# Kernel tuning notes

Hardware: AMD Instinct MI355X
Metric: run time of the kernel (lower is better)

The kernel has to match this reference:

```python
import jax, jax.numpy as jnp
import numpy as np

T, B, D, H, DEPTH = 256, 64, 1024, 1024, 2


def setup_inputs() -> dict:
    key = jax.random.key(0)
    ks = jax.random.split(key, 12)
    s_in = (1.0 / (D + H)) ** 0.5  # torch Linear default init scale
    s_h = (1.0 / H) ** 0.5
    qc_v = jax.random.uniform(ks[9], (DEPTH, H, H), jnp.float32, -s_h, s_h)
    # weight_norm init: g = ||v|| per output row, so initial w == v
    qc_g = jnp.linalg.norm(qc_v, axis=2)
    return {
        "inputs": jax.random.normal(ks[0], (T, B, D), jnp.float32),
        "Wf": jax.random.uniform(ks[1], (H, D + H), jnp.float32, -s_in, s_in),
        "bf": jax.random.uniform(ks[2], (H,), jnp.float32, -s_in, s_in),
        "Wi": jax.random.uniform(ks[3], (H, D + H), jnp.float32, -s_in, s_in),
        "bi": jax.random.uniform(ks[4], (H,), jnp.float32, -s_in, s_in),
        "Wu": jax.random.uniform(ks[5], (H, D + H), jnp.float32, -s_in, s_in),
        "bu": jax.random.uniform(ks[6], (H,), jnp.float32, -s_in, s_in),
        "Wo": jax.random.uniform(ks[7], (H, D + H), jnp.float32, -s_in, s_in),
        "bo": jax.random.uniform(ks[8], (H,), jnp.float32, -s_in, s_in),
        "qc_v": qc_v,
        "qc_g": qc_g,
        "qc_b": jax.random.uniform(ks[10], (DEPTH, H), jnp.float32, -s_h, s_h),
    }


def reference(inputs, Wf, bf, Wi, bi, Wu, bu, Wo, bo, qc_v, qc_g, qc_b):
    # weight_norm (dim=0): w = g * v / ||v||_row
    qc_w = qc_g[:, :, None] * qc_v / jnp.linalg.norm(qc_v, axis=2, keepdims=True)

    def qc(x):  # x: [4, B, H] -> tanh(linear) applied DEPTH times (shared across gates)
        for d in range(DEPTH):
            x = jnp.tanh(jnp.einsum('gbh,oh->gbo', x, qc_w[d]) + qc_b[d])
        return x

    h0 = jnp.zeros((inputs.shape[1], bf.shape[0]), inputs.dtype)

    def step(carry, x):
        hx, cx = carry
        comb = jnp.concatenate([x, hx], axis=1)  # [B, D+H]
        f = jax.nn.sigmoid(comb @ Wf.T + bf)
        i = jax.nn.sigmoid(comb @ Wi.T + bi)
        g = jnp.tanh(comb @ Wu.T + bu)
        o = jax.nn.sigmoid(comb @ Wo.T + bo)
        f, i, g, o = qc(jnp.stack([f, i, g, o]))
        cx = f * cx + i * g
        hx = o * jnp.tanh(cx)
        return (hx, cx), hx

    (hx, cx), outputs = jax.lax.scan(step, (h0, h0), inputs)
    return outputs, hx, cx
```

## Files before the change

kernel.cpp:

```cpp
#include <hip/hip_runtime.h>
#include <cstdint>
#include <cstddef>

typedef float f32x4 __attribute__((ext_vector_type(4)));
typedef __bf16 bf16x8 __attribute__((ext_vector_type(8)));
typedef unsigned int u32x4 __attribute__((ext_vector_type(4)));

#define T_STEPS 256
#define HD      1024
#define DHK     2048

#define LDSW_BYTES (32 * 256 * 16)
#define LDS_TOTAL  (LDSW_BYTES + 4 * 16 * 68 * 4)

__device__ __forceinline__ unsigned short f2bf(float f) {
  union { float f; unsigned u; } v; v.f = f;
  unsigned r = v.u + 0x7fffu + ((v.u >> 16) & 1u);
  return (unsigned short)(r >> 16);
}

__device__ __forceinline__ float fast_sigmoid(float x) {
  return 1.0f / (1.0f + __expf(-x));
}
__device__ __forceinline__ float fast_tanh(float x) {
  float e = __expf(2.0f * x);
  return (e - 1.0f) / (e + 1.0f);
}

__device__ __forceinline__ f32x4 mfma16(bf16x8 a, bf16x8 b, f32x4 c) {
  return __builtin_amdgcn_mfma_f32_16x16x32_bf16(a, b, c, 0, 0, 0);
}

#define LOADC(dst, vofs, base, IMM)                                            \
  asm volatile("global_load_dwordx4 %0, %1, %2 offset:" IMM " sc0 sc1"         \
               : "=v"(dst) : "v"(vofs), "s"(base) : "memory")

#define L8(st, vofs, base)                                                     \
  LOADC(st[0], vofs, base, "0");   LOADC(st[1], vofs, base, "64");             \
  LOADC(st[2], vofs, base, "128"); LOADC(st[3], vofs, base, "192");            \
  LOADC(st[4], vofs, base, "256"); LOADC(st[5], vofs, base, "320");            \
  LOADC(st[6], vofs, base, "384"); LOADC(st[7], vofs, base, "448")

#define WAITV0()                                                               \
  do { asm volatile("s_waitcnt vmcnt(0)" ::: "memory");                        \
       __builtin_amdgcn_sched_barrier(0); } while (0)

__device__ __forceinline__ void storec8(void* p, ushort4 v) {
  asm volatile("global_store_dwordx2 %0, %1, off sc0 sc1"
               :: "v"(p), "v"(v) : "memory");
}
__device__ __forceinline__ void storec2(void* p, unsigned short v) {
  unsigned vv = v;
  asm volatile("global_store_short %0, %1, off sc0 sc1"
               :: "v"(p), "v"(vv) : "memory");
}

__device__ __forceinline__ void release_flag(int* f, int v) {
  asm volatile("s_waitcnt vmcnt(0)" ::: "memory");
  __hip_atomic_store(f, v, __ATOMIC_RELAXED, __HIP_MEMORY_SCOPE_AGENT);
}
__device__ __forceinline__ void wait_ge(const int* f, int v) {
  while (__hip_atomic_load(f, __ATOMIC_RELAXED, __HIP_MEMORY_SCOPE_AGENT) < v)
    __builtin_amdgcn_s_sleep(1);
  asm volatile("" ::: "memory");
}

__global__ __launch_bounds__(256, 1) void qlstm_persist(
    const unsigned short* __restrict__ Xbf,
    const unsigned short* __restrict__ Wbf,
    const unsigned short* __restrict__ qcw,
    const float* __restrict__ bias_cat,
    const float* __restrict__ qcb,
    unsigned short* __restrict__ Gbf,
    unsigned short* __restrict__ G2bf,
    unsigned short* __restrict__ hbf,
    float* __restrict__ c_state,
    float* __restrict__ out,
    int* __restrict__ aA, int* __restrict__ aB, int* __restrict__ aC) {
  extern __shared__ char lds_raw[];
  uint4* lw = (uint4*)lds_raw;
  float* red = (float*)(lds_raw + LDSW_BYTES);

  const int nb = blockIdx.x, tid = threadIdx.x;
  const int wv = tid >> 6, lane = tid & 63;
  const int l15 = lane & 15, l16 = lane >> 4;
  const int l16o = l16 * 8;
  const int q = nb >> 6;
  const int n0 = (nb & 63) * 16;
  const int kb = wv * 256;

  {
    const unsigned short* wArow = Wbf + (size_t)(nb * 16 + l15) * DHK + kb + l16o;
    const unsigned short* wBrow = qcw + (size_t)(n0 + l15) * HD + kb + l16o;
    const unsigned short* wCrow = wBrow + (size_t)HD * HD;
#pragma unroll
    for (int s = 0; s < 8; ++s) {
      lw[s * 256 + tid]        = *(const uint4*)&wArow[s * 32];
      lw[(8 + s) * 256 + tid]  = *(const uint4*)&wArow[1024 + s * 32];
      lw[(16 + s) * 256 + tid] = *(const uint4*)&wBrow[s * 32];
      lw[(24 + s) * 256 + tid] = *(const uint4*)&wCrow[s * 32];
    }
  }
  __syncthreads();

  const int erow = tid >> 2, ecb = (tid & 3) * 4;
  const int bl = tid >> 4, cc = tid & 15;
  f32x4 biasA, biasB;
#pragma unroll
  for (int i = 0; i < 4; ++i) {
    biasA[i] = bias_cat[nb * 16 + ecb + i];
    biasB[i] = qcb[n0 + ecb + i];
  }
  const float biasC = qcb[HD + n0 + cc];

  int vofsAB[4], vofsC[4];
#pragma unroll
  for (int mt = 0; mt < 4; ++mt) {
    vofsAB[mt] = ((mt * 16 + l15) * HD + kb + l16o) * 2;
    vofsC[mt]  = ((mt * 64 + q * 16 + l15) * HD + kb + l16o) * 2;
  }
  const unsigned short* hB = hbf;
  const unsigned short* gB = Gbf + (size_t)(q * 64) * HD;

  for (int t = 0; t < T_STEPS; ++t) {
    {
      f32x4 acc[4] = {};
      const unsigned short* xb = Xbf + (size_t)t * (64 * HD);
#pragma unroll
      for (int s = 0; s < 8; ++s) {
        bf16x8 w = *(const bf16x8*)&lw[s * 256 + tid];
#pragma unroll
        for (int mt = 0; mt < 4; ++mt) {
          bf16x8 a =
              *(const bf16x8*)&xb[(size_t)(mt * 16 + l15) * HD + kb + s * 32 + l16o];
          acc[mt] = mfma16(a, w, acc[mt]);
        }
      }
      wait_ge(&aC[tid], t);
      __syncthreads();
      {
        bf16x8 st0[8], st1[8], st2[8], st3[8];
        L8(st0, vofsAB[0], hB); L8(st1, vofsAB[1], hB);
        L8(st2, vofsAB[2], hB); L8(st3, vofsAB[3], hB);
        WAITV0();
#pragma unroll
        for (int s = 0; s < 8; ++s) {
          bf16x8 w = *(const bf16x8*)&lw[(8 + s) * 256 + tid];
          acc[0] = mfma16(st0[s], w, acc[0]);
          acc[1] = mfma16(st1[s], w, acc[1]);
          acc[2] = mfma16(st2[s], w, acc[2]);
          acc[3] = mfma16(st3[s], w, acc[3]);
        }
      }
#pragma unroll
      for (int mt = 0; mt < 4; ++mt)
        *(f32x4*)&red[(wv * 16 + l15) * 68 + mt * 16 + l16 * 4] = acc[mt];
      __syncthreads();
      ushort4 pk;
#pragma unroll
      for (int i = 0; i < 4; ++i) {
        const int c = ecb + i;
        float v = red[(0 * 16 + c) * 68 + erow] + red[(1 * 16 + c) * 68 + erow] +
                  red[(2 * 16 + c) * 68 + erow] + red[(3 * 16 + c) * 68 + erow] +
                  biasA[i];
        v = (q == 2) ? fast_tanh(v) : fast_sigmoid(v);
        ((unsigned short*)&pk)[i] = f2bf(v);
      }
      storec8(&Gbf[(size_t)(q * 64 + erow) * HD + n0 + ecb], pk);
      __syncthreads();
      if (tid == 0) release_flag(&aA[nb], t + 1);
    }
    {
      if (tid < 64) wait_ge(&aA[q * 64 + tid], t + 1);
      __syncthreads();
      f32x4 acc[4] = {};
      {
        bf16x8 st0[8], st1[8], st2[8], st3[8];
        L8(st0, vofsAB[0], gB); L8(st1, vofsAB[1], gB);
        L8(st2, vofsAB[2], gB); L8(st3, vofsAB[3], gB);
        WAITV0();
#pragma unroll
        for (int s = 0; s < 8; ++s) {
          bf16x8 w = *(const bf16x8*)&lw[(16 + s) * 256 + tid];
          acc[0] = mfma16(st0[s], w, acc[0]);
          acc[1] = mfma16(st1[s], w, acc[1]);
          acc[2] = mfma16(st2[s], w, acc[2]);
          acc[3] = mfma16(st3[s], w, acc[3]);
        }
      }
#pragma unroll
      for (int mt = 0; mt < 4; ++mt)
        *(f32x4*)&red[(wv * 16 + l15) * 68 + mt * 16 + l16 * 4] = acc[mt];
      __syncthreads();
      ushort4 pk;
#pragma unroll
      for (int i = 0; i < 4; ++i) {
        const int c = ecb + i;
        float v = red[(0 * 16 + c) * 68 + erow] + red[(1 * 16 + c) * 68 + erow] +
                  red[(2 * 16 + c) * 68 + erow] + red[(3 * 16 + c) * 68 + erow] +
                  biasB[i];
        ((unsigned short*)&pk)[i] = f2bf(fast_tanh(v));
      }
      storec8(&G2bf[(size_t)(q * 64 + erow) * HD + n0 + ecb], pk);
      __syncthreads();
      if (tid == 0) release_flag(&aB[nb], t + 1);
    }
    {
      wait_ge(&aB[tid], t + 1);
      __syncthreads();
      f32x4 acc[4] = {};
      {
        bf16x8 st0[8], st1[8], st2[8], st3[8];
        L8(st0, vofsC[0], G2bf); L8(st1, vofsC[1], G2bf);
        L8(st2, vofsC[2], G2bf); L8(st3, vofsC[3], G2bf);
        WAITV0();
#pragma unroll
        for (int s = 0; s < 8; ++s) {
          bf16x8 w = *(const bf16x8*)&lw[(24 + s) * 256 + tid];
          acc[0] = mfma16(st0[s], w, acc[0]);
          acc[1] = mfma16(st1[s], w, acc[1]);
          acc[2] = mfma16(st2[s], w, acc[2]);
          acc[3] = mfma16(st3[s], w, acc[3]);
        }
      }
#pragma unroll
      for (int mt = 0; mt < 4; ++mt)
        *(f32x4*)&red[(wv * 16 + l15) * 68 + mt * 16 + l16 * 4] = acc[mt];
      __syncthreads();
      float gv[4];
#pragma unroll
      for (int g = 0; g < 4; ++g) {
        const int r = g * 16 + bl;
        float v = red[(0 * 16 + cc) * 68 + r] + red[(1 * 16 + cc) * 68 + r] +
                  red[(2 * 16 + cc) * 68 + r] + red[(3 * 16 + cc) * 68 + r] +
                  biasC;
        gv[g] = fast_tanh(v);
      }
      const int ci = (q * 16 + bl) * HD + n0 + cc;
      const float c_new = gv[0] * c_state[ci] + gv[1] * gv[2];
      const float h_new = gv[3] * fast_tanh(c_new);
      c_state[ci] = c_new;
      out[(size_t)t * (64 * HD) + ci] = h_new;
      storec2(&hbf[ci], f2bf(h_new));
      if (t == T_STEPS - 1) {
        out[(size_t)T_STEPS * (64 * HD) + ci] = h_new;
        out[(size_t)T_STEPS * (64 * HD) + 64 * HD + ci] = c_new;
      }
      __syncthreads();
      if (tid == 0) release_flag(&aC[nb], t + 1);
    }
  }
}

__global__ void xconv_kernel(const float* __restrict__ x,
                             unsigned short* __restrict__ xbf, int n4) {
  int idx = blockIdx.x * blockDim.x + threadIdx.x;
  int stride = gridDim.x * blockDim.x;
  for (int i = idx; i < n4; i += stride) {
    float4 v = ((const float4*)x)[i];
    ushort4 o;
    o.x = f2bf(v.x); o.y = f2bf(v.y); o.z = f2bf(v.z); o.w = f2bf(v.w);
    ((ushort4*)xbf)[i] = o;
  }
}

__global__ void wconv_kernel(const float* __restrict__ Wf, const float* __restrict__ Wi,
                             const float* __restrict__ Wu, const float* __restrict__ Wo,
                             const float* __restrict__ bfv, const float* __restrict__ biv,
                             const float* __restrict__ buv, const float* __restrict__ bov,
                             unsigned short* __restrict__ Wbf, float* __restrict__ bias_cat) {
  const int n = blockIdx.x;
  const int gate = n >> 10, r = n & 1023;
  const float* W = gate == 0 ? Wf : gate == 1 ? Wi : gate == 2 ? Wu : Wo;
  const float* src = W + (size_t)r * DHK;
  unsigned short* dst = Wbf + (size_t)n * DHK;
  for (int k = threadIdx.x; k < DHK; k += 256) dst[k] = f2bf(src[k]);
  if (threadIdx.x == 0) {
    const float* bsrc = gate == 0 ? bfv : gate == 1 ? biv : gate == 2 ? buv : bov;
    bias_cat[n] = bsrc[r];
  }
}

__global__ void qcw_kernel(const float* __restrict__ qcv, const float* __restrict__ qcg,
                           unsigned short* __restrict__ qcw) {
  const int row = blockIdx.x * 4 + (threadIdx.x >> 6);
  const int lane = threadIdx.x & 63;
  const float* v = qcv + (size_t)row * HD;
  float ss = 0.0f;
#pragma unroll
  for (int j = 0; j < 16; ++j) { float a = v[j * 64 + lane]; ss += a * a; }
#pragma unroll
  for (int off = 32; off > 0; off >>= 1) ss += __shfl_xor(ss, off);
  const float scale = qcg[row] / sqrtf(ss);
#pragma unroll
  for (int j = 0; j < 16; ++j)
    qcw[(size_t)row * HD + j * 64 + lane] = f2bf(v[j * 64 + lane] * scale);
}

__global__ void init_state_kernel(unsigned short* __restrict__ hbf,
                                  float* __restrict__ c_state,
                                  int* __restrict__ flags) {
  int i = blockIdx.x * blockDim.x + threadIdx.x;
  hbf[i] = 0;
  c_state[i] = 0.0f;
  if (i < 768) flags[i] = 0;
}

extern "C" void kernel_launch(void* const* d_in, const int* in_sizes, int n_in,
                              void* d_out, int out_size, void* d_ws, size_t ws_size,
                              hipStream_t stream) {
  const float* x   = (const float*)d_in[0];
  const float* Wf  = (const float*)d_in[1];
  const float* bfv = (const float*)d_in[2];
  const float* Wi  = (const float*)d_in[3];
  const float* biv = (const float*)d_in[4];
  const float* Wu  = (const float*)d_in[5];
  const float* buv = (const float*)d_in[6];
  const float* Wo  = (const float*)d_in[7];
  const float* bov = (const float*)d_in[8];
  const float* qcv = (const float*)d_in[9];
  const float* qcg = (const float*)d_in[10];
  const float* qcb = (const float*)d_in[11];
  float* out = (float*)d_out;

  char* p = (char*)d_ws;
  auto alloc = [&](size_t bytes) {
    char* r = p; p += (bytes + 255) & ~(size_t)255; return r;
  };
  unsigned short* Xbf  = (unsigned short*)alloc((size_t)T_STEPS * 64 * HD * 2);
  unsigned short* Wbf  = (unsigned short*)alloc((size_t)4096 * DHK * 2);
  unsigned short* qcw  = (unsigned short*)alloc((size_t)2 * HD * HD * 2);
  float* bias_cat      = (float*)alloc((size_t)4096 * 4);
  unsigned short* Gbf  = (unsigned short*)alloc((size_t)256 * HD * 2);
  unsigned short* G2bf = (unsigned short*)alloc((size_t)256 * HD * 2);
  unsigned short* hbf  = (unsigned short*)alloc((size_t)64 * HD * 2);
  float* c_state       = (float*)alloc((size_t)64 * HD * 4);
  int* flags           = (int*)alloc(768 * 4);

  static int lds_set = 0;
  if (!lds_set) {
    hipFuncSetAttribute((const void*)qlstm_persist,
                        hipFuncAttributeMaxDynamicSharedMemorySize, LDS_TOTAL);
    lds_set = 1;
  }

  init_state_kernel<<<256, 256, 0, stream>>>(hbf, c_state, flags);
  xconv_kernel<<<2048, 256, 0, stream>>>(x, Xbf, T_STEPS * 64 * HD / 4);
  wconv_kernel<<<4096, 256, 0, stream>>>(Wf, Wi, Wu, Wo, bfv, biv, buv, bov,
                                         Wbf, bias_cat);
  qcw_kernel<<<512, 256, 0, stream>>>(qcv, qcg, qcw);

  qlstm_persist<<<256, 256, LDS_TOTAL, stream>>>(
      Xbf, Wbf, qcw, bias_cat, qcb, Gbf, G2bf, hbf, c_state, out,
      flags, flags + 256, flags + 512);
}
```

Measured before the change: 6.637 ms.

## Replace per-block flags with atomic counters, prefetch x-projection, keep cell state in registers

```diff
diff --git a/kernel.cpp b/kernel.cpp
--- a/kernel.cpp
+++ b/kernel.cpp
@@ -4,7 +4,6 @@
 
 typedef float f32x4 __attribute__((ext_vector_type(4)));
 typedef __bf16 bf16x8 __attribute__((ext_vector_type(8)));
-typedef unsigned int u32x4 __attribute__((ext_vector_type(4)));
 
 #define T_STEPS 256
 #define HD      1024
@@ -55,12 +54,12 @@
                :: "v"(p), "v"(vv) : "memory");
 }
 
-__device__ __forceinline__ void release_flag(int* f, int v) {
-  asm volatile("s_waitcnt vmcnt(0)" ::: "memory");
-  __hip_atomic_store(f, v, __ATOMIC_RELAXED, __HIP_MEMORY_SCOPE_AGENT);
-}
-__device__ __forceinline__ void wait_ge(const int* f, int v) {
-  while (__hip_atomic_load(f, __ATOMIC_RELAXED, __HIP_MEMORY_SCOPE_AGENT) < v)
+__device__ __forceinline__ void bump(int* cnt) {
+  __hip_atomic_fetch_add(cnt, 1, __ATOMIC_RELAXED, __HIP_MEMORY_SCOPE_AGENT);
+}
+__device__ __forceinline__ void wait_cnt(const int* cnt, int target) {
+  while (__hip_atomic_load(cnt, __ATOMIC_RELAXED, __HIP_MEMORY_SCOPE_AGENT) <
+         target)
     __builtin_amdgcn_s_sleep(1);
   asm volatile("" ::: "memory");
 }
@@ -74,9 +73,8 @@
     unsigned short* __restrict__ Gbf,
     unsigned short* __restrict__ G2bf,
     unsigned short* __restrict__ hbf,
-    float* __restrict__ c_state,
     float* __restrict__ out,
-    int* __restrict__ aA, int* __restrict__ aB, int* __restrict__ aC) {
+    int* __restrict__ cnt) {
   extern __shared__ char lds_raw[];
   uint4* lw = (uint4*)lds_raw;
   float* red = (float*)(lds_raw + LDSW_BYTES);
@@ -88,6 +86,7 @@
   const int q = nb >> 6;
   const int n0 = (nb & 63) * 16;
   const int kb = wv * 256;
+  int* cntA = cnt, * cntB = cnt + 1, * cntC = cnt + 2;
 
   {
     const unsigned short* wArow = Wbf + (size_t)(nb * 16 + l15) * DHK + kb + l16o;
@@ -112,6 +111,7 @@
     biasB[i] = qcb[n0 + ecb + i];
   }
   const float biasC = qcb[HD + n0 + cc];
+  const int ci = (q * 16 + bl) * HD + n0 + cc;
 
   int vofsAB[4], vofsC[4];
 #pragma unroll
@@ -122,21 +122,31 @@
   const unsigned short* hB = hbf;
   const unsigned short* gB = Gbf + (size_t)(q * 64) * HD;
 
+  float c_reg = 0.0f;
+  f32x4 accA[4];
+
+#define XPRELUDE(tt)                                                           \
+  do {                                                                         \
+    const unsigned short* xb = Xbf + (size_t)(tt) * (64 * HD);                 \
+    _Pragma("unroll")                                                          \
+    for (int mt = 0; mt < 4; ++mt) accA[mt] = (f32x4){0.f, 0.f, 0.f, 0.f};     \
+    _Pragma("unroll")                                                          \
+    for (int s = 0; s < 8; ++s) {                                              \
+      bf16x8 w = *(const bf16x8*)&lw[s * 256 + tid];                           \
+      _Pragma("unroll")                                                        \
+      for (int mt = 0; mt < 4; ++mt) {                                         \
+        bf16x8 a = *(const bf16x8*)&xb[(size_t)(mt * 16 + l15) * HD + kb +     \
+                                       s * 32 + l16o];                         \
+        accA[mt] = mfma16(a, w, accA[mt]);                                     \
+      }                                                                        \
+    }                                                                          \
+  } while (0)
+
+  XPRELUDE(0);
+
   for (int t = 0; t < T_STEPS; ++t) {
     {
-      f32x4 acc[4] = {};
-      const unsigned short* xb = Xbf + (size_t)t * (64 * HD);
-#pragma unroll
-      for (int s = 0; s < 8; ++s) {
-        bf16x8 w = *(const bf16x8*)&lw[s * 256 + tid];
-#pragma unroll
-        for (int mt = 0; mt < 4; ++mt) {
-          bf16x8 a =
-              *(const bf16x8*)&xb[(size_t)(mt * 16 + l15) * HD + kb + s * 32 + l16o];
-          acc[mt] = mfma16(a, w, acc[mt]);
-        }
-      }
-      wait_ge(&aC[tid], t);
+      if (tid == 0) wait_cnt(cntC, 256 * t);
       __syncthreads();
       {
         bf16x8 st0[8], st1[8], st2[8], st3[8];
@@ -146,15 +156,15 @@
 #pragma unroll
         for (int s = 0; s < 8; ++s) {
           bf16x8 w = *(const bf16x8*)&lw[(8 + s) * 256 + tid];
-          acc[0] = mfma16(st0[s], w, acc[0]);
-          acc[1] = mfma16(st1[s], w, acc[1]);
-          acc[2] = mfma16(st2[s], w, acc[2]);
-          acc[3] = mfma16(st3[s], w, acc[3]);
+          accA[0] = mfma16(st0[s], w, accA[0]);
+          accA[1] = mfma16(st1[s], w, accA[1]);
+          accA[2] = mfma16(st2[s], w, accA[2]);
+          accA[3] = mfma16(st3[s], w, accA[3]);
         }
       }
 #pragma unroll
       for (int mt = 0; mt < 4; ++mt)
-        *(f32x4*)&red[(wv * 16 + l15) * 68 + mt * 16 + l16 * 4] = acc[mt];
+        *(f32x4*)&red[(wv * 16 + l15) * 68 + mt * 16 + l16 * 4] = accA[mt];
       __syncthreads();
       ushort4 pk;
 #pragma unroll
@@ -168,10 +178,11 @@
       }
       storec8(&Gbf[(size_t)(q * 64 + erow) * HD + n0 + ecb], pk);
       __syncthreads();
-      if (tid == 0) release_flag(&aA[nb], t + 1);
+      if (tid == 0) bump(cntA);
     }
+    if (t + 1 < T_STEPS) XPRELUDE(t + 1);
     {
-      if (tid < 64) wait_ge(&aA[q * 64 + tid], t + 1);
+      if (tid == 0) wait_cnt(cntA, 256 * (t + 1));
       __syncthreads();
       f32x4 acc[4] = {};
       {
@@ -203,10 +214,10 @@
       }
       storec8(&G2bf[(size_t)(q * 64 + erow) * HD + n0 + ecb], pk);
       __syncthreads();
-      if (tid == 0) release_flag(&aB[nb], t + 1);
+      if (tid == 0) bump(cntB);
     }
     {
-      wait_ge(&aB[tid], t + 1);
+      if (tid == 0) wait_cnt(cntB, 256 * (t + 1));
       __syncthreads();
       f32x4 acc[4] = {};
       {
@@ -236,18 +247,17 @@
                   biasC;
         gv[g] = fast_tanh(v);
       }
-      const int ci = (q * 16 + bl) * HD + n0 + cc;
-      const float c_new = gv[0] * c_state[ci] + gv[1] * gv[2];
+      const float c_new = gv[0] * c_reg + gv[1] * gv[2];
       const float h_new = gv[3] * fast_tanh(c_new);
-      c_state[ci] = c_new;
+      c_reg = c_new;
+      storec2(&hbf[ci], f2bf(h_new));
+      __syncthreads();
+      if (tid == 0) bump(cntC);
       out[(size_t)t * (64 * HD) + ci] = h_new;
-      storec2(&hbf[ci], f2bf(h_new));
       if (t == T_STEPS - 1) {
         out[(size_t)T_STEPS * (64 * HD) + ci] = h_new;
         out[(size_t)T_STEPS * (64 * HD) + 64 * HD + ci] = c_new;
       }
-      __syncthreads();
-      if (tid == 0) release_flag(&aC[nb], t + 1);
     }
   }
 }
@@ -298,12 +308,10 @@
 }
 
 __global__ void init_state_kernel(unsigned short* __restrict__ hbf,
-                                  float* __restrict__ c_state,
-                                  int* __restrict__ flags) {
+                                  int* __restrict__ cnt) {
   int i = blockIdx.x * blockDim.x + threadIdx.x;
   hbf[i] = 0;
-  c_state[i] = 0.0f;
-  if (i < 768) flags[i] = 0;
+  if (i < 3) cnt[i] = 0;
 }
 
 extern "C" void kernel_launch(void* const* d_in, const int* in_sizes, int n_in,
@@ -334,8 +342,7 @@
   unsigned short* Gbf  = (unsigned short*)alloc((size_t)256 * HD * 2);
   unsigned short* G2bf = (unsigned short*)alloc((size_t)256 * HD * 2);
   unsigned short* hbf  = (unsigned short*)alloc((size_t)64 * HD * 2);
-  float* c_state       = (float*)alloc((size_t)64 * HD * 4);
-  int* flags           = (int*)alloc(768 * 4);
+  int* cnt             = (int*)alloc(256);
 
   static int lds_set = 0;
   if (!lds_set) {
@@ -344,13 +351,12 @@
     lds_set = 1;
   }
 
-  init_state_kernel<<<256, 256, 0, stream>>>(hbf, c_state, flags);
+  init_state_kernel<<<256, 256, 0, stream>>>(hbf, cnt);
   xconv_kernel<<<2048, 256, 0, stream>>>(x, Xbf, T_STEPS * 64 * HD / 4);
   wconv_kernel<<<4096, 256, 0, stream>>>(Wf, Wi, Wu, Wo, bfv, biv, buv, bov,
                                          Wbf, bias_cat);
   qcw_kernel<<<512, 256, 0, stream>>>(qcv, qcg, qcw);
 
   qlstm_persist<<<256, 256, LDS_TOTAL, stream>>>(
-      Xbf, Wbf, qcw, bias_cat, qcb, Gbf, G2bf, hbf, c_state, out,
-      flags, flags + 256, flags + 512);
-}
+      Xbf, Wbf, qcw, bias_cat, qcb, Gbf, G2bf, hbf, out, cnt);
+}
```

Result: slower. 7.354 ms (+10.8%).
